# Optimization experiments

Hardware: AMD Instinct MI355X
Metric: run time of the kernel (lower is better)

The kernel has to match this reference:

```python
import jax, jax.numpy as jnp
import numpy as np

B, N, D = 32, 50000, 64  # batch, node_num, num_inputs


def setup_inputs() -> dict:
    key = jax.random.key(0)
    k1, k2, k3 = jax.random.split(key, 3)
    x = jax.random.normal(k1, (B, N, D), dtype=jnp.float32)
    # xavier_uniform_ with gain=1.414 on a (2D, 1) matrix: bound = gain*sqrt(6/(fan_in+fan_out))
    bound = 1.414 * np.sqrt(6.0 / (2 * D + 1))
    a = jax.random.uniform(k2, (2 * D, 1), minval=-bound, maxval=bound, dtype=jnp.float32)
    adj_mask = jax.random.randint(k3, (N,), 0, 2).astype(jnp.int32)
    node_index = 123  # scalar target-node index
    return {"x": x, "a": a, "node_index": node_index, "adj_mask": adj_mask}


def reference(x, a, node_index, adj_mask):
    # torch: concat([x[:, idx].expand(node_num), x], -1) @ a  ==  x[:, idx] @ a[:D] + x @ a[D:]
    d = x.shape[-1]
    a_tgt = a[:d, 0]   # weights applied to the (broadcast) target-node features
    a_src = a[d:, 0]   # weights applied to every node's own features
    tgt_score = x[:, node_index] @ a_tgt          # [B]
    e = jax.nn.leaky_relu(tgt_score[:, None] + x @ a_src, negative_slope=0.01)  # [B, N]
    neg = jnp.asarray(-9e15, e.dtype)
    masked = jnp.where(adj_mask > 0, e, neg)
    attention = jax.nn.softmax(masked, axis=1) * adj_mask.astype(e.dtype)[None, :]
    return attention
```

## Files before the change

### kernel.cpp

```cpp
#include <hip/hip_runtime.h>

#define NN 50000
#define DD 64
#define BB 32

__global__ __launch_bounds__(256) void attn_pass1(
    const float* __restrict__ x, const float* __restrict__ a,
    const int* __restrict__ node_index, const int* __restrict__ adj,
    float* __restrict__ out, float* __restrict__ sums)
{
    const int tid = threadIdx.x;
    const int b = blockIdx.y;
    const int node = *node_index;

    __shared__ float sh_tgt;
    __shared__ float sh_part[4];

    if (tid < 64) {
        float v = x[(size_t)b * NN * DD + (size_t)node * DD + tid] * a[tid];
        #pragma unroll
        for (int o = 32; o >= 1; o >>= 1) v += __shfl_xor(v, o, 64);
        if (tid == 0) sh_tgt = v;
    }
    __syncthreads();
    const float tgt = sh_tgt;

    const int wave = tid >> 6;
    const int lane = tid & 63;
    const int g = lane >> 4;
    const int c = lane & 15;

    const float4 av = ((const float4*)(a + DD))[c];

    float local = 0.f;
    const int rowBase = blockIdx.x * 256;
    const float* xb = x + (size_t)b * NN * DD;

    #pragma unroll 4
    for (int i = 0; i < 16; i++) {
        const int row = rowBase + i * 16 + wave * 4 + g;
        const bool valid = (row < NN);
        const int msk = valid ? adj[row] : 0;

        float s = 0.f;
        if (msk > 0) {
            const float4 xv = ((const float4*)(xb + (size_t)row * DD))[c];
            s = xv.x * av.x + xv.y * av.y + xv.z * av.z + xv.w * av.w;
        }
        s += __shfl_xor(s, 1, 64);
        s += __shfl_xor(s, 2, 64);
        s += __shfl_xor(s, 4, 64);
        s += __shfl_xor(s, 8, 64);

        if (c == 0 && valid) {
            float p = 0.f;
            if (msk > 0) {
                const float z = tgt + s;
                const float e = (z > 0.f) ? z : 0.01f * z;
                p = __expf(e);
            }
            out[(size_t)b * NN + row] = p;
            local += p;
        }
    }

    #pragma unroll
    for (int o = 32; o >= 1; o >>= 1) local += __shfl_xor(local, o, 64);
    if (lane == 0) sh_part[wave] = local;
    __syncthreads();
    if (tid == 0)
        atomicAdd(&sums[b], sh_part[0] + sh_part[1] + sh_part[2] + sh_part[3]);
}

__global__ __launch_bounds__(256) void attn_pass2(
    float* __restrict__ out, const float* __restrict__ sums)
{
    const int N4 = NN / 4;
    const int f = blockIdx.x * blockDim.x + threadIdx.x;
    const int b = blockIdx.y;
    if (f < N4) {
        const float inv = 1.0f / sums[b];
        float4* p = (float4*)out + (size_t)b * N4 + f;
        float4 v = *p;
        v.x *= inv; v.y *= inv; v.z *= inv; v.w *= inv;
        *p = v;
    }
}

extern "C" void kernel_launch(void* const* d_in, const int* in_sizes, int n_in,
                              void* d_out, int out_size, void* d_ws, size_t ws_size,
                              hipStream_t stream) {
    const float* x = (const float*)d_in[0];
    const float* a = (const float*)d_in[1];
    const int* node_index = (const int*)d_in[2];
    const int* adj = (const int*)d_in[3];
    float* out = (float*)d_out;
    float* sums = (float*)d_ws;

    hipMemsetAsync(sums, 0, BB * sizeof(float), stream);

    dim3 g1((NN + 255) / 256, BB);
    attn_pass1<<<g1, 256, 0, stream>>>(x, a, node_index, adj, out, sums);

    dim3 g2((NN / 4 + 255) / 256, BB);
    attn_pass2<<<g2, 256, 0, stream>>>(out, sums);
}
```

Baseline: 550.5 us.

## Fuse softmax passes into one cooperative kernel with LDS-stashed exponentials

Merges the exp/sum pass and the normalization pass into a single cooperative kernel. Each block handles a 1568-row chunk, keeps the exponentials in shared memory, writes per-block partial sums, does a grid-wide sync, then writes the normalized output once. This removes the memset, the atomics, the second launch and the re-read and re-write of the output. In exchange the grid shrinks to 1024 blocks of 256 threads, which lowers the number of loads in flight for streaming x, and it adds a grid barrier.

```diff
diff --git a/kernel.cpp b/kernel.cpp
--- a/kernel.cpp
+++ b/kernel.cpp
@@ -1,20 +1,28 @@
 #include <hip/hip_runtime.h>
+#include <hip/hip_cooperative_groups.h>
+namespace cg = cooperative_groups;
 
 #define NN 50000
 #define DD 64
 #define BB 32
+#define CHUNKS 32
+#define RPB 1568
+#define ITERS (RPB / 16)
 
-__global__ __launch_bounds__(256) void attn_pass1(
+__global__ __launch_bounds__(256) void attn_fused(
     const float* __restrict__ x, const float* __restrict__ a,
     const int* __restrict__ node_index, const int* __restrict__ adj,
-    float* __restrict__ out, float* __restrict__ sums)
+    float* __restrict__ out, float* __restrict__ pbs )
 {
     const int tid = threadIdx.x;
+    const int chunk = blockIdx.x;
     const int b = blockIdx.y;
     const int node = *node_index;
 
+    __shared__ float p_stash[RPB];
     __shared__ float sh_tgt;
     __shared__ float sh_part[4];
+    __shared__ float sh_inv;
 
     if (tid < 64) {
         float v = x[(size_t)b * NN * DD + (size_t)node * DD + tid] * a[tid];
@@ -31,14 +39,13 @@
     const int c = lane & 15;
 
     const float4 av = ((const float4*)(a + DD))[c];
+    const int rowBase = chunk * RPB;
+    const float* xb = x + (size_t)b * NN * DD;
 
     float local = 0.f;
-    const int rowBase = blockIdx.x * 256;
-    const float* xb = x + (size_t)b * NN * DD;
-
-    #pragma unroll 4
-    for (int i = 0; i < 16; i++) {
-        const int row = rowBase + i * 16 + wave * 4 + g;
+    for (int i = 0; i < ITERS; i++) {
+        const int lrow = i * 16 + wave * 4 + g;
+        const int row = rowBase + lrow;
         const bool valid = (row < NN);
         const int msk = valid ? adj[row] : 0;
 
@@ -52,14 +59,14 @@
         s += __shfl_xor(s, 4, 64);
         s += __shfl_xor(s, 8, 64);
 
-        if (c == 0 && valid) {
+        if (c == 0) {
             float p = 0.f;
             if (msk > 0) {
                 const float z = tgt + s;
                 const float e = (z > 0.f) ? z : 0.01f * z;
                 p = __expf(e);
             }
-            out[(size_t)b * NN + row] = p;
+            p_stash[lrow] = p;
             local += p;
         }
     }
@@ -69,21 +76,23 @@
     if (lane == 0) sh_part[wave] = local;
     __syncthreads();
     if (tid == 0)
-        atomicAdd(&sums[b], sh_part[0] + sh_part[1] + sh_part[2] + sh_part[3]);
-}
+        pbs[b * CHUNKS + chunk] = sh_part[0] + sh_part[1] + sh_part[2] + sh_part[3];
 
-__global__ __launch_bounds__(256) void attn_pass2(
-    float* __restrict__ out, const float* __restrict__ sums)
-{
-    const int N4 = NN / 4;
-    const int f = blockIdx.x * blockDim.x + threadIdx.x;
-    const int b = blockIdx.y;
-    if (f < N4) {
-        const float inv = 1.0f / sums[b];
-        float4* p = (float4*)out + (size_t)b * N4 + f;
-        float4 v = *p;
-        v.x *= inv; v.y *= inv; v.z *= inv; v.w *= inv;
-        *p = v;
+    __threadfence();
+    cg::this_grid().sync();
+
+    if (tid < 32) {
+        float v = pbs[b * CHUNKS + tid];
+        #pragma unroll
+        for (int o = 16; o >= 1; o >>= 1) v += __shfl_xor(v, o, 64);
+        if (tid == 0) sh_inv = 1.0f / v;
+    }
+    __syncthreads();
+    const float inv = sh_inv;
+
+    for (int li = tid; li < RPB; li += 256) {
+        const int row = rowBase + li;
+        if (row < NN) out[(size_t)b * NN + row] = p_stash[li] * inv;
     }
 }
 
@@ -95,13 +104,11 @@
     const int* node_index = (const int*)d_in[2];
     const int* adj = (const int*)d_in[3];
     float* out = (float*)d_out;
-    float* sums = (float*)d_ws;
+    float* pbs = (float*)d_ws;
 
-    hipMemsetAsync(sums, 0, BB * sizeof(float), stream);
-
-    dim3 g1((NN + 255) / 256, BB);
-    attn_pass1<<<g1, 256, 0, stream>>>(x, a, node_index, adj, out, sums);
-
-    dim3 g2((NN / 4 + 255) / 256, BB);
-    attn_pass2<<<g2, 256, 0, stream>>>(out, sums);
+    void* args[] = { (void*)&x, (void*)&a, (void*)&node_index, (void*)&adj,
+                     (void*)&out, (void*)&pbs };
+    dim3 grid(CHUNKS, BB);
+    dim3 block(256);
+    hipLaunchCooperativeKernel((void*)attn_fused, grid, block, args, 0, stream);
 }
```

Result: slower. 792.1 us (+43.9%).

## Stage adjacency mask in LDS, batch row loads, coalesce probability writes

Applied to the files above, without the earlier changes.

Loads the adjacency mask for the tile into shared memory once, and has each wave handle a contiguous 64-row chunk. Each lane issues eight independent float4 loads before reducing them, which raises memory-level parallelism. Probabilities are staged in shared memory and written out as one coalesced 256-wide store instead of scattered single-lane writes. This costs more registers and some shared memory, which may lower occupancy.

```diff
diff --git a/kernel.cpp b/kernel.cpp
--- a/kernel.cpp
+++ b/kernel.cpp
@@ -3,6 +3,7 @@
 #define NN 50000
 #define DD 64
 #define BB 32
+#define TILE 256
 
 __global__ __launch_bounds__(256) void attn_pass1(
     const float* __restrict__ x, const float* __restrict__ a,
@@ -11,10 +12,18 @@
 {
     const int tid = threadIdx.x;
     const int b = blockIdx.y;
+    const int rowBase = blockIdx.x * TILE;
     const int node = *node_index;
 
+    __shared__ int   sh_adj[TILE];
+    __shared__ float sh_p[TILE];
     __shared__ float sh_tgt;
     __shared__ float sh_part[4];
+
+    {
+        const int r = rowBase + tid;
+        sh_adj[tid] = (r < NN) ? adj[r] : 0;
+    }
 
     if (tid < 64) {
         float v = x[(size_t)b * NN * DD + (size_t)node * DD + tid] * a[tid];
@@ -31,36 +40,43 @@
     const int c = lane & 15;
 
     const float4 av = ((const float4*)(a + DD))[c];
+    const float* xb = x + (size_t)b * NN * DD;
 
     float local = 0.f;
-    const int rowBase = blockIdx.x * 256;
-    const float* xb = x + (size_t)b * NN * DD;
 
-    #pragma unroll 4
-    for (int i = 0; i < 16; i++) {
-        const int row = rowBase + i * 16 + wave * 4 + g;
-        const bool valid = (row < NN);
-        const int msk = valid ? adj[row] : 0;
-
-        float s = 0.f;
-        if (msk > 0) {
-            const float4 xv = ((const float4*)(xb + (size_t)row * DD))[c];
-            s = xv.x * av.x + xv.y * av.y + xv.z * av.z + xv.w * av.w;
+    #pragma unroll
+    for (int h = 0; h < 2; h++) {
+        int   msk[8];
+        float4 xv[8];
+        #pragma unroll
+        for (int u = 0; u < 8; u++) {
+            const int lrow = wave * 64 + h * 32 + u * 4 + g;
+            msk[u] = sh_adj[lrow];
+            if (msk[u] > 0) {
+                const size_t row = (size_t)(rowBase + lrow);
+                xv[u] = ((const float4*)(xb + row * DD))[c];
+            } else {
+                xv[u] = make_float4(0.f, 0.f, 0.f, 0.f);
+            }
         }
-        s += __shfl_xor(s, 1, 64);
-        s += __shfl_xor(s, 2, 64);
-        s += __shfl_xor(s, 4, 64);
-        s += __shfl_xor(s, 8, 64);
-
-        if (c == 0 && valid) {
-            float p = 0.f;
-            if (msk > 0) {
-                const float z = tgt + s;
-                const float e = (z > 0.f) ? z : 0.01f * z;
-                p = __expf(e);
+        #pragma unroll
+        for (int u = 0; u < 8; u++) {
+            float s = xv[u].x * av.x + xv[u].y * av.y + xv[u].z * av.z + xv[u].w * av.w;
+            s += __shfl_xor(s, 1, 64);
+            s += __shfl_xor(s, 2, 64);
+            s += __shfl_xor(s, 4, 64);
+            s += __shfl_xor(s, 8, 64);
+            if (c == 0) {
+                const int lrow = wave * 64 + h * 32 + u * 4 + g;
+                float p = 0.f;
+                if (msk[u] > 0) {
+                    const float z = tgt + s;
+                    const float e = (z > 0.f) ? z : 0.01f * z;
+                    p = __expf(e);
+                }
+                sh_p[lrow] = p;
+                local += p;
             }
-            out[(size_t)b * NN + row] = p;
-            local += p;
         }
     }
 
@@ -70,6 +86,11 @@
     __syncthreads();
     if (tid == 0)
         atomicAdd(&sums[b], sh_part[0] + sh_part[1] + sh_part[2] + sh_part[3]);
+
+    {
+        const int r = rowBase + tid;
+        if (r < NN) out[(size_t)b * NN + r] = sh_p[tid];
+    }
 }
 
 __global__ __launch_bounds__(256) void attn_pass2(
@@ -99,7 +120,7 @@
 
     hipMemsetAsync(sums, 0, BB * sizeof(float), stream);
 
-    dim3 g1((NN + 255) / 256, BB);
+    dim3 g1((NN + TILE - 1) / TILE, BB);
     attn_pass1<<<g1, 256, 0, stream>>>(x, a, node_index, adj, out, sums);
 
     dim3 g2((NN / 4 + 255) / 256, BB);
```

Measured after the change: 506.8 us. -7.9%, faster.
